# Performance work log

Hardware: AMD Instinct MI355X
Metric: run time of the kernel (lower is better)

## Reference

```python
import jax, jax.numpy as jnp
import numpy as np

NUM_HEADS = 8
D_MODEL = 512
QKV = 512
OUT = 512
B, T = 8, 1024
W = 2 * T - 1  # relative position range


def _relative_shift(x):
    # x: [B, H, T, 2T-1] -> [B, H, T, T] (Transformer-XL shift trick)
    b, h, t, w = x.shape
    zero_pad = jnp.zeros((b, h, t, 1), dtype=x.dtype)
    x = jnp.concatenate([zero_pad, x], axis=-1)  # [B,H,T,2T]
    x = x.reshape(b, h, 2 * t, t)
    x = x[:, :, 1:, :]
    x = x.reshape(b, h, t, 2 * t - 1)
    return x[:, :, :, :t]


def setup_inputs() -> dict:
    key = jax.random.key(0)
    ks = jax.random.split(key, 12)
    s_in = 1.0 / np.sqrt(D_MODEL)
    s_qkv = 1.0 / np.sqrt(QKV)
    return {
        "x": jax.random.normal(ks[0], (B, T, D_MODEL), jnp.float32),
        "pos_emb": jax.random.normal(ks[1], (W, D_MODEL), jnp.float32),
        "Wq": jax.random.normal(ks[2], (D_MODEL, QKV), jnp.float32) * s_in,
        "bq": jnp.zeros((QKV,), jnp.float32),
        "Wk": jax.random.normal(ks[3], (D_MODEL, QKV), jnp.float32) * s_in,
        "Wv": jax.random.normal(ks[4], (D_MODEL, QKV), jnp.float32) * s_in,
        "Wp": jax.random.normal(ks[5], (D_MODEL, QKV), jnp.float32) * s_in,
        "Wo": jax.random.normal(ks[6], (QKV, OUT), jnp.float32) * s_qkv,
        "bo": jnp.zeros((OUT,), jnp.float32),
        "u": jax.random.normal(ks[7], (NUM_HEADS, QKV // NUM_HEADS), jnp.float32),
        "v": jax.random.normal(ks[8], (NUM_HEADS, QKV // NUM_HEADS), jnp.float32),
    }


def reference(x, pos_emb, Wq, bq, Wk, Wv, Wp, Wo, bo, u, v):
    b, t, _ = x.shape
    h = NUM_HEADS
    d = Wq.shape[1] // h
    q = (x @ Wq + bq).reshape(b, t, h, d)
    k = (x @ Wk).reshape(b, t, h, d)
    val = (x @ Wv).reshape(b, t, h, d)
    p = (pos_emb @ Wp).reshape(-1, h, d)  # [2T-1, H, d]

    # content scores: (q + u) . k  -> [B,H,T,T]
    content_scores = jnp.einsum('bthd,bshd->bhts', q + u, k)
    # position scores: (q + v) . p -> [B,H,T,2T-1], then relative shift
    pos_scores = jnp.einsum('bthd,whd->bhtw', q + v, p)
    pos_scores = _relative_shift(pos_scores)

    scores = (content_scores + pos_scores) / jnp.sqrt(jnp.asarray(d, x.dtype))
    probs = jax.nn.softmax(scores, axis=-1)
    attn_out = jnp.einsum('bhts,bshd->bthd', probs, val).reshape(b, t, h * d)
    return attn_out @ Wo + bo
```

## Files before the change

kernel.cpp:

```cpp
#include <hip/hip_runtime.h>
#include <hip/hip_bf16.h>


typedef __attribute__((ext_vector_type(8))) short short8;
typedef __attribute__((ext_vector_type(4))) float float4v;
typedef __fp16 h2v __attribute__((ext_vector_type(2)));

__device__ __forceinline__ unsigned short f2bf(float f) {
  union { float f; unsigned u; } x; x.f = f;
  unsigned r = x.u + 0x7FFFu + ((x.u >> 16) & 1u);
  return (unsigned short)(r >> 16);
}
__device__ __forceinline__ float bf2f(unsigned short b) {
  union { unsigned u; float f; } x; x.u = ((unsigned)b) << 16;
  return x.f;
}
__device__ __forceinline__ int pk2h(float a, float b) {
  union { h2v h; int i; } c; c.h = __builtin_amdgcn_cvt_pkrtz(a, b);
  return c.i;
}
__device__ __forceinline__ float h_lo(int w) {
  union { int i; h2v h; } c; c.i = w; return (float)c.h.x;
}
__device__ __forceinline__ float h_hi(int w) {
  union { int i; h2v h; } c; c.i = w; return (float)c.h.y;
}

__global__ void cvt_bf16_kernel(const float* __restrict__ in,
                                unsigned short* __restrict__ out, int n4) {
  int i = blockIdx.x * blockDim.x + threadIdx.x;
  if (i < n4) {
    float4 f = ((const float4*)in)[i];
    ushort4 r;
    r.x = f2bf(f.x); r.y = f2bf(f.y); r.z = f2bf(f.z); r.w = f2bf(f.w);
    ((ushort4*)out)[i] = r;
  }
}

__global__ void transpose_cvt5_kernel(const float* __restrict__ Wq,
                                      const float* __restrict__ Wk,
                                      const float* __restrict__ Wv,
                                      const float* __restrict__ Wp,
                                      const float* __restrict__ Wo,
                                      unsigned short* __restrict__ dst) {
  int y = blockIdx.y;
  const float* w = (y == 0) ? Wq : (y == 1) ? Wk : (y == 2) ? Wv : (y == 3) ? Wp : Wo;
  unsigned short* wt = dst + (size_t)y * 262144;
  int idx = blockIdx.x * 256 + threadIdx.x;
  int kk = idx >> 9, n = idx & 511;
  wt[(n << 9) | kk] = f2bf(w[idx]);
}

__global__ __launch_bounds__(256, 2) void qkv_gemm128(
    const unsigned short* __restrict__ A,
    const unsigned short* __restrict__ Bt,
    const float* __restrict__ bq,
    const float* __restrict__ uvec,
    const float* __restrict__ vvec,
    unsigned short* __restrict__ QU, unsigned short* __restrict__ QV,
    unsigned short* __restrict__ Kb, unsigned short* __restrict__ Vt) {
  __shared__ __align__(16) unsigned short lds[2 * 128 * 72];
  unsigned short (*As)[72] = (unsigned short(*)[72])lds;
  unsigned short (*Bs)[72] = (unsigned short(*)[72])(lds + 128 * 72);
  int mt = blockIdx.x, nt = blockIdx.y;
  int tid = threadIdx.x;
  int lane = tid & 63, wave = tid >> 6;
  int l15 = lane & 15, g = lane >> 4;
  int wr = (wave >> 1) << 6, wc = (wave & 1) << 6;
  int sr = tid >> 1, sc = (tid & 1) << 5;

  const unsigned short* Ap = A + (size_t)(mt * 128 + sr) * 512 + sc;
  const unsigned short* Bp = Bt + (size_t)(nt * 128 + sr) * 512 + sc;

  uint4 a0 = *(const uint4*)Ap,        a1 = *(const uint4*)(Ap + 8);
  uint4 a2 = *(const uint4*)(Ap + 16), a3 = *(const uint4*)(Ap + 24);
  uint4 b0 = *(const uint4*)Bp,        b1 = *(const uint4*)(Bp + 8);
  uint4 b2 = *(const uint4*)(Bp + 16), b3 = *(const uint4*)(Bp + 24);

  float4v acc[4][4] = {};
  for (int kt = 0; kt < 8; ++kt) {
    *(uint4*)&As[sr][sc]      = a0; *(uint4*)&As[sr][sc + 8]  = a1;
    *(uint4*)&As[sr][sc + 16] = a2; *(uint4*)&As[sr][sc + 24] = a3;
    *(uint4*)&Bs[sr][sc]      = b0; *(uint4*)&Bs[sr][sc + 8]  = b1;
    *(uint4*)&Bs[sr][sc + 16] = b2; *(uint4*)&Bs[sr][sc + 24] = b3;
    __syncthreads();
    if (kt < 7) {
      const unsigned short* ap = Ap + (kt + 1) * 64;
      a0 = *(const uint4*)ap;        a1 = *(const uint4*)(ap + 8);
      a2 = *(const uint4*)(ap + 16); a3 = *(const uint4*)(ap + 24);
      const unsigned short* bp = Bp + (kt + 1) * 64;
      b0 = *(const uint4*)bp;        b1 = *(const uint4*)(bp + 8);
      b2 = *(const uint4*)(bp + 16); b3 = *(const uint4*)(bp + 24);
    }
#pragma unroll
    for (int ks = 0; ks < 2; ++ks) {
      short8 af[4], bf[4];
#pragma unroll
      for (int fm = 0; fm < 4; ++fm)
        af[fm] = *(const short8*)&As[wr + fm * 16 + l15][ks * 32 + g * 8];
#pragma unroll
      for (int fn = 0; fn < 4; ++fn)
        bf[fn] = *(const short8*)&Bs[wc + fn * 16 + l15][ks * 32 + g * 8];
#pragma unroll
      for (int fm = 0; fm < 4; ++fm)
#pragma unroll
        for (int fn = 0; fn < 4; ++fn)
          acc[fm][fn] = __builtin_amdgcn_mfma_f32_16x16x32_bf16(
              af[fm], bf[fn], acc[fm][fn], 0, 0, 0);
    }
    if (kt < 7) __syncthreads();
  }

  if (nt < 4) {
#pragma unroll
    for (int fn = 0; fn < 4; ++fn) {
      int col = nt * 128 + wc + fn * 16 + l15;
      float bs = bq[col], uu = uvec[col], vv = vvec[col];
#pragma unroll
      for (int fm = 0; fm < 4; ++fm) {
        int row = mt * 128 + wr + fm * 16 + 4 * g;
#pragma unroll
        for (int r = 0; r < 4; ++r) {
          size_t idx = (size_t)(row + r) * 512 + col;
          float base = acc[fm][fn][r] + bs;
          QU[idx] = f2bf(base + uu);
          QV[idx] = f2bf(base + vv);
        }
      }
    }
  } else if (nt < 8) {
#pragma unroll
    for (int fn = 0; fn < 4; ++fn) {
      int col = (nt - 4) * 128 + wc + fn * 16 + l15;
#pragma unroll
      for (int fm = 0; fm < 4; ++fm) {
        int row = mt * 128 + wr + fm * 16 + 4 * g;
#pragma unroll
        for (int r = 0; r < 4; ++r)
          Kb[(size_t)(row + r) * 512 + col] = f2bf(acc[fm][fn][r]);
      }
    }
  } else {
    __syncthreads();
    unsigned short (*T)[136] = (unsigned short(*)[136])lds;
#pragma unroll
    for (int fm = 0; fm < 4; ++fm)
#pragma unroll
      for (int fn = 0; fn < 4; ++fn)
#pragma unroll
        for (int r = 0; r < 4; ++r)
          T[wc + fn * 16 + l15][wr + fm * 16 + 4 * g + r] = f2bf(acc[fm][fn][r]);
    __syncthreads();
    int c2 = tid >> 1, sh = (tid & 1) << 6;
    int gcol = (nt - 8) * 128 + c2;
    int bb = mt >> 3, s0 = (mt & 7) * 128;
    unsigned short* op = Vt +
        ((size_t)((bb * 8 + (gcol >> 6)) * 64 + (gcol & 63))) * 1024 + s0 + sh;
#pragma unroll
    for (int j = 0; j < 8; ++j)
      *(uint4*)(op + j * 8) = *(uint4*)&T[c2][sh + j * 8];
  }
}

__global__ __launch_bounds__(256, 2) void gemm128f(
    const unsigned short* __restrict__ A,
    const unsigned short* __restrict__ Bt,
    const float* __restrict__ bias,
    float* __restrict__ Cf) {
  __shared__ __align__(16) unsigned short lds[2 * 128 * 72];
  unsigned short (*As)[72] = (unsigned short(*)[72])lds;
  unsigned short (*Bs)[72] = (unsigned short(*)[72])(lds + 128 * 72);
  int mt = blockIdx.x, nt = blockIdx.y;
  int tid = threadIdx.x;
  int lane = tid & 63, wave = tid >> 6;
  int l15 = lane & 15, g = lane >> 4;
  int wr = (wave >> 1) << 6, wc = (wave & 1) << 6;
  int sr = tid >> 1, sc = (tid & 1) << 5;

  const unsigned short* Ap = A + (size_t)(mt * 128 + sr) * 512 + sc;
  const unsigned short* Bp = Bt + (size_t)(nt * 128 + sr) * 512 + sc;

  uint4 a0 = *(const uint4*)Ap,        a1 = *(const uint4*)(Ap + 8);
  uint4 a2 = *(const uint4*)(Ap + 16), a3 = *(const uint4*)(Ap + 24);
  uint4 b0 = *(const uint4*)Bp,        b1 = *(const uint4*)(Bp + 8);
  uint4 b2 = *(const uint4*)(Bp + 16), b3 = *(const uint4*)(Bp + 24);

  float4v acc[4][4] = {};
  for (int kt = 0; kt < 8; ++kt) {
    *(uint4*)&As[sr][sc]      = a0; *(uint4*)&As[sr][sc + 8]  = a1;
    *(uint4*)&As[sr][sc + 16] = a2; *(uint4*)&As[sr][sc + 24] = a3;
    *(uint4*)&Bs[sr][sc]      = b0; *(uint4*)&Bs[sr][sc + 8]  = b1;
    *(uint4*)&Bs[sr][sc + 16] = b2; *(uint4*)&Bs[sr][sc + 24] = b3;
    __syncthreads();
    if (kt < 7) {
      const unsigned short* ap = Ap + (kt + 1) * 64;
      a0 = *(const uint4*)ap;        a1 = *(const uint4*)(ap + 8);
      a2 = *(const uint4*)(ap + 16); a3 = *(const uint4*)(ap + 24);
      const unsigned short* bp = Bp + (kt + 1) * 64;
      b0 = *(const uint4*)bp;        b1 = *(const uint4*)(bp + 8);
      b2 = *(const uint4*)(bp + 16); b3 = *(const uint4*)(bp + 24);
    }
#pragma unroll
    for (int ks = 0; ks < 2; ++ks) {
      short8 af[4], bf[4];
#pragma unroll
      for (int fm = 0; fm < 4; ++fm)
        af[fm] = *(const short8*)&As[wr + fm * 16 + l15][ks * 32 + g * 8];
#pragma unroll
      for (int fn = 0; fn < 4; ++fn)
        bf[fn] = *(const short8*)&Bs[wc + fn * 16 + l15][ks * 32 + g * 8];
#pragma unroll
      for (int fm = 0; fm < 4; ++fm)
#pragma unroll
        for (int fn = 0; fn < 4; ++fn)
          acc[fm][fn] = __builtin_amdgcn_mfma_f32_16x16x32_bf16(
              af[fm], bf[fn], acc[fm][fn], 0, 0, 0);
    }
    if (kt < 7) __syncthreads();
  }
#pragma unroll
  for (int fn = 0; fn < 4; ++fn) {
    int col = nt * 128 + wc + fn * 16 + l15;
    float bs = bias[col];
#pragma unroll
    for (int fm = 0; fm < 4; ++fm) {
      int row = mt * 128 + wr + fm * 16 + 4 * g;
#pragma unroll
      for (int r = 0; r < 4; ++r)
        Cf[(size_t)(row + r) * 512 + col] = acc[fm][fn][r] + bs;
    }
  }
}

__global__ __launch_bounds__(256) void gemm_kernel(
    const unsigned short* __restrict__ A,
    const unsigned short* __restrict__ Bt,
    const float* __restrict__ bias,
    unsigned short* __restrict__ Cb,
    float* __restrict__ Cf,
    int M, int f32out) {
  __shared__ __align__(16) unsigned short As[64][72];
  __shared__ __align__(16) unsigned short Bs[64][72];
  int mt = blockIdx.x, nt = blockIdx.y;
  int tid = threadIdx.x;
  int lr = tid >> 2, lc = (tid & 3) << 4;
  int lane = tid & 63, wave = tid >> 6;

  int arow = mt * 64 + lr; if (arow >= M) arow = M - 1;
  const unsigned short* Ap = A + (size_t)arow * 512 + lc;
  const unsigned short* Bp = Bt + (size_t)(nt * 64 + lr) * 512 + lc;

  uint4 a0 = *(const uint4*)Ap, a1 = *(const uint4*)(Ap + 8);
  uint4 b0 = *(const uint4*)Bp, b1 = *(const uint4*)(Bp + 8);
  float4v acc[4] = {};
  for (int kt = 0; kt < 8; ++kt) {
    *(uint4*)&As[lr][lc]     = a0;
    *(uint4*)&As[lr][lc + 8] = a1;
    *(uint4*)&Bs[lr][lc]     = b0;
    *(uint4*)&Bs[lr][lc + 8] = b1;
    __syncthreads();
    if (kt < 7) {
      a0 = *(const uint4*)(Ap + (kt + 1) * 64);
      a1 = *(const uint4*)(Ap + (kt + 1) * 64 + 8);
      b0 = *(const uint4*)(Bp + (kt + 1) * 64);
      b1 = *(const uint4*)(Bp + (kt + 1) * 64 + 8);
    }
#pragma unroll
    for (int ks = 0; ks < 2; ++ks) {
      short8 a = *(const short8*)&As[wave * 16 + (lane & 15)][ks * 32 + (lane >> 4) * 8];
#pragma unroll
      for (int fn = 0; fn < 4; ++fn) {
        short8 b = *(const short8*)&Bs[fn * 16 + (lane & 15)][ks * 32 + (lane >> 4) * 8];
        acc[fn] = __builtin_amdgcn_mfma_f32_16x16x32_bf16(a, b, acc[fn], 0, 0, 0);
      }
    }
    if (kt < 7) __syncthreads();
  }
  int rbase = mt * 64 + wave * 16 + ((lane >> 4) << 2);
  int cb = nt * 64 + (lane & 15);
#pragma unroll
  for (int fn = 0; fn < 4; ++fn) {
    int col = cb + fn * 16;
    float bs = bias ? bias[col] : 0.0f;
#pragma unroll
    for (int r = 0; r < 4; ++r) {
      int row = rbase + r;
      if (row < M) {
        float val = acc[fn][r] + bs;
        if (f32out) Cf[(size_t)row * 512 + col] = val;
        else        Cb[(size_t)row * 512 + col] = f2bf(val);
      }
    }
  }
}

__global__ __launch_bounds__(256, 3) void attn_kernel(
    const unsigned short* __restrict__ QU,
    const unsigned short* __restrict__ QV,
    const unsigned short* __restrict__ K,
    const unsigned short* __restrict__ Vt,
    const unsigned short* __restrict__ P,
    unsigned short* __restrict__ O) {
  __shared__ __align__(16) unsigned short k_s[64][72];
  __shared__ __align__(16) unsigned short vt_s[64][72];
  __shared__ __align__(16) unsigned short win_s[128 * 72];

  int pid = blockIdx.x;
  int wid = (pid & 7) * 128 + (pid >> 3);
  int tt = wid & 15, h = (wid >> 4) & 7, b = wid >> 7;
  int t0 = tt * 64;
  int tid = threadIdx.x, lane = tid & 63, wave = tid >> 6;
  int lr = tid >> 2, lc = (tid & 3) << 4;
  int l15 = lane & 15, g = lane >> 4;
  int w16 = wave * 16;
  int C = 3 - wave;

  short8 aqu[2], aqv[2];
  {
    size_t qoff = (size_t)(b * 1024 + t0 + w16 + l15) * 512 + h * 64 + g * 8;
    aqu[0] = *(const short8*)(QU + qoff);
    aqu[1] = *(const short8*)(QU + qoff + 32);
    aqv[0] = *(const short8*)(QV + qoff);
    aqv[1] = *(const short8*)(QV + qoff + 32);
  }

  const unsigned short* Kbase = K + (size_t)(b * 1024) * 512 + h * 64;
  const unsigned short* Vbase = Vt + (size_t)((b * 8 + h) * 64) * 1024;

  float4v accO[4] = {};
  float l_r[4] = {0.f, 0.f, 0.f, 0.f};

  {
    const unsigned short* kp = Kbase + (size_t)lr * 512 + lc;
    uint4 k0 = *(const uint4*)kp, k1 = *(const uint4*)(kp + 8);
    const unsigned short* vp = Vbase + (size_t)lr * 1024 + lc;
    uint4 v0 = *(const uint4*)vp, v1 = *(const uint4*)(vp + 8);
    int r2 = tid >> 1, c2 = (tid & 1) << 5;
    int ph0 = (tt + 1) & 1;
    int wr = 960 - t0 + r2;
    const unsigned short* pp = P + (size_t)wr * 512 + h * 64 + c2;
    uint4 w0v = *(const uint4*)pp,        w1v = *(const uint4*)(pp + 8);
    uint4 w2v = *(const uint4*)(pp + 16), w3v = *(const uint4*)(pp + 24);
    *(uint4*)&k_s[lr][lc]      = k0; *(uint4*)&k_s[lr][lc + 8]  = k1;
    *(uint4*)&vt_s[lr][lc]     = v0; *(uint4*)&vt_s[lr][lc + 8] = v1;
    unsigned short* dp = &win_s[(r2 ^ (ph0 << 6)) * 72 + c2];
    *(uint4*)dp        = w0v; *(uint4*)(dp + 8)  = w1v;
    *(uint4*)(dp + 16) = w2v; *(uint4*)(dp + 24) = w3v;
  }
  __syncthreads();

  uint4 pk0, pk1, pv0, pv1, pw0, pw1;
  for (int st = 0; st < 16; ++st) {
    int ph = (st + tt + 1) & 1;
    if (st < 15) {
      int s0n = (st + 1) * 64;
      const unsigned short* kp = Kbase + (size_t)(s0n + lr) * 512 + lc;
      pk0 = *(const uint4*)kp; pk1 = *(const uint4*)(kp + 8);
      const unsigned short* vp = Vbase + (size_t)lr * 1024 + s0n + lc;
      pv0 = *(const uint4*)vp; pv1 = *(const uint4*)(vp + 8);
      int wr = 64 * st - t0 + 1088 + lr; if (wr > 2046) wr = 2046;
      const unsigned short* pp = P + (size_t)wr * 512 + h * 64 + lc;
      pw0 = *(const uint4*)pp; pw1 = *(const uint4*)(pp + 8);
    }

    float4v accS[4] = {}; float4v accP[5] = {};
#pragma unroll
    for (int ks = 0; ks < 2; ++ks) {
#pragma unroll
      for (int fn = 0; fn < 4; ++fn) {
        short8 bk = *(const short8*)&k_s[fn * 16 + l15][ks * 32 + g * 8];
        accS[fn] = __builtin_amdgcn_mfma_f32_16x16x32_bf16(aqu[ks], bk, accS[fn], 0, 0, 0);
      }
#pragma unroll
      for (int k = 0; k < 5; ++k) {
        int fi = (k + C) ^ (ph << 2);
        short8 bp = *(const short8*)&win_s[(fi * 16 + l15) * 72 + ks * 32 + g * 8];
        accP[k] = __builtin_amdgcn_mfma_f32_16x16x32_bf16(aqv[ks], bp, accP[k], 0, 0, 0);
      }
    }

#pragma unroll
    for (int r = 0; r < 4; ++r) {
      int W0 = pk2h(accP[0][r], accP[1][r]);
      int W1 = pk2h(accP[1][r], accP[2][r]);
      int W2 = pk2h(accP[2][r], accP[3][r]);
      int W3 = pk2h(accP[3][r], accP[4][r]);
      int srcLane = (lane & 48) | ((l15 - 4 * g - r - 1) & 15);
      int carry = (l15 >= 4 * g + r + 1);
      int x0 = __shfl(W0, srcLane), x1 = __shfl(W1, srcLane);
      int x2 = __shfl(W2, srcLane), x3 = __shfl(W3, srcLane);
      int wa = carry ? x1 : x0;
      int wb = carry ? x3 : x2;
      accS[0][r] = (accS[0][r] + h_lo(wa)) * 0.125f;
      accS[1][r] = (accS[1][r] + h_hi(wa)) * 0.125f;
      accS[2][r] = (accS[2][r] + h_lo(wb)) * 0.125f;
      accS[3][r] = (accS[3][r] + h_hi(wb)) * 0.125f;
    }

    __syncthreads();

    int pbase = (ph << 6) + w16;
#pragma unroll
    for (int r = 0; r < 4; ++r) {
      float rs = 0.f;
#pragma unroll
      for (int fn = 0; fn < 4; ++fn) {
        float e = __expf(accS[fn][r] - 8.0f);
        win_s[(pbase + 4 * g + r) * 72 + fn * 16 + l15] = f2bf(e);
        rs += e;
      }
      l_r[r] += rs;
    }

#pragma unroll
    for (int ks = 0; ks < 2; ++ks) {
      short8 ap = *(const short8*)&win_s[(pbase + l15) * 72 + ks * 32 + g * 8];
#pragma unroll
      for (int fn = 0; fn < 4; ++fn) {
        short8 bv = *(const short8*)&vt_s[fn * 16 + l15][ks * 32 + g * 8];
        accO[fn] = __builtin_amdgcn_mfma_f32_16x16x32_bf16(ap, bv, accO[fn], 0, 0, 0);
      }
    }

    if (st < 15) {
      __syncthreads();
      *(uint4*)&k_s[lr][lc]      = pk0; *(uint4*)&k_s[lr][lc + 8]  = pk1;
      *(uint4*)&vt_s[lr][lc]     = pv0; *(uint4*)&vt_s[lr][lc + 8] = pv1;
      unsigned short* dp = &win_s[(lr + (ph << 6)) * 72 + lc];
      *(uint4*)dp = pw0; *(uint4*)(dp + 8) = pw1;
      __syncthreads();
    }
  }

  float rinv[4];
#pragma unroll
  for (int r = 0; r < 4; ++r) {
    float l = l_r[r];
    l += __shfl_xor(l, 1); l += __shfl_xor(l, 2);
    l += __shfl_xor(l, 4); l += __shfl_xor(l, 8);
    rinv[r] = 1.0f / l;
  }
#pragma unroll
  for (int fn = 0; fn < 4; ++fn) {
    int dcol = fn * 16 + l15;
#pragma unroll
    for (int r = 0; r < 4; ++r) {
      int row = t0 + w16 + 4 * g + r;
      float o = accO[fn][r] * rinv[r];
      O[(size_t)(b * 1024 + row) * 512 + h * 64 + dcol] = f2bf(o);
    }
  }
}

extern "C" void kernel_launch(void* const* d_in, const int* in_sizes, int n_in,
                              void* d_out, int out_size, void* d_ws, size_t ws_size,
                              hipStream_t stream) {
  const float* x       = (const float*)d_in[0];
  const float* pos_emb = (const float*)d_in[1];
  const float* Wq      = (const float*)d_in[2];
  const float* bq      = (const float*)d_in[3];
  const float* Wk      = (const float*)d_in[4];
  const float* Wv      = (const float*)d_in[5];
  const float* Wp      = (const float*)d_in[6];
  const float* Wo      = (const float*)d_in[7];
  const float* bo      = (const float*)d_in[8];
  const float* u       = (const float*)d_in[9];
  const float* v       = (const float*)d_in[10];

  char* ws = (char*)d_ws;
  unsigned short* xb   = (unsigned short*)ws; ws += (size_t)8192 * 512 * 2;
  unsigned short* peb  = (unsigned short*)ws; ws += (size_t)2048 * 512 * 2;
  unsigned short* wqkv = (unsigned short*)ws; ws += (size_t)5 * 512 * 512 * 2;
  unsigned short* qub  = (unsigned short*)ws; ws += (size_t)8192 * 512 * 2;
  unsigned short* qvb  = (unsigned short*)ws; ws += (size_t)8192 * 512 * 2;
  unsigned short* kb   = (unsigned short*)ws; ws += (size_t)8192 * 512 * 2;
  unsigned short* vtb  = (unsigned short*)ws; ws += (size_t)8192 * 512 * 2;
  unsigned short* pb   = (unsigned short*)ws; ws += (size_t)2048 * 512 * 2;
  unsigned short* attb = (unsigned short*)ws; ws += (size_t)8192 * 512 * 2;

  cvt_bf16_kernel<<<4096, 256, 0, stream>>>(x, xb, 1048576);
  cvt_bf16_kernel<<<1024, 256, 0, stream>>>(pos_emb, peb, 262016);
  transpose_cvt5_kernel<<<dim3(1024, 5), 256, 0, stream>>>(Wq, Wk, Wv, Wp, Wo, wqkv);
  unsigned short* wpt_p = wqkv + (size_t)3 * 262144;
  unsigned short* wot_p = wqkv + (size_t)4 * 262144;

  qkv_gemm128<<<dim3(64, 12), 256, 0, stream>>>(xb, wqkv, bq, u, v,
                                                qub, qvb, kb, vtb);
  gemm_kernel<<<dim3(32, 8), 256, 0, stream>>>(peb, wpt_p, nullptr, pb, nullptr, 2047, 0);

  attn_kernel<<<1024, 256, 0, stream>>>(qub, qvb, kb, vtb, pb, attb);

  gemm128f<<<dim3(64, 4), 256, 0, stream>>>(attb, wot_p, bo, (float*)d_out);
}
```

Before: 128.5 us.

## Double attention query tile, fuse position GEMM into QKV GEMM, tile weight transpose

The attention kernel now processes 128 query rows per block as two 64-row subtiles. The K/V tiles and a larger 192-row position window are shared across both subtiles, halving K/V reloads and the number of blocks. The position embedding projection is folded into the QKV GEMM launch as an extra grid row, removing a separate kernel launch. The weight transpose uses an LDS tile for coalesced reads and writes. The cost is higher register and LDS use per block in attention, which lowers occupancy.

```diff
diff --git a/kernel.cpp b/kernel.cpp
--- a/kernel.cpp
+++ b/kernel.cpp
@@ -10,10 +10,6 @@
   union { float f; unsigned u; } x; x.f = f;
   unsigned r = x.u + 0x7FFFu + ((x.u >> 16) & 1u);
   return (unsigned short)(r >> 16);
-}
-__device__ __forceinline__ float bf2f(unsigned short b) {
-  union { unsigned u; float f; } x; x.u = ((unsigned)b) << 16;
-  return x.f;
 }
 __device__ __forceinline__ int pk2h(float a, float b) {
   union { h2v h; int i; } c; c.h = __builtin_amdgcn_cvt_pkrtz(a, b);
@@ -43,12 +39,28 @@
                                       const float* __restrict__ Wp,
                                       const float* __restrict__ Wo,
                                       unsigned short* __restrict__ dst) {
+  __shared__ float T[64][65];
   int y = blockIdx.y;
   const float* w = (y == 0) ? Wq : (y == 1) ? Wk : (y == 2) ? Wv : (y == 3) ? Wp : Wo;
   unsigned short* wt = dst + (size_t)y * 262144;
-  int idx = blockIdx.x * 256 + threadIdx.x;
-  int kk = idx >> 9, n = idx & 511;
-  wt[(n << 9) | kk] = f2bf(w[idx]);
+  int bx = blockIdx.x;
+  int r0 = (bx >> 3) * 64, c0 = (bx & 7) * 64;
+  int tid = threadIdx.x;
+  int row = tid >> 2, cq = (tid & 3) * 16;
+  const float* src = w + (size_t)(r0 + row) * 512 + c0 + cq;
+#pragma unroll
+  for (int j = 0; j < 4; ++j) {
+    float4 f = *(const float4*)(src + j * 4);
+    T[row][cq + j * 4 + 0] = f.x; T[row][cq + j * 4 + 1] = f.y;
+    T[row][cq + j * 4 + 2] = f.z; T[row][cq + j * 4 + 3] = f.w;
+  }
+  __syncthreads();
+  unsigned short tmp[16];
+#pragma unroll
+  for (int j = 0; j < 16; ++j) tmp[j] = f2bf(T[cq + j][row]);
+  unsigned short* op = wt + (size_t)(c0 + row) * 512 + r0 + cq;
+  *(uint4*)op       = *(uint4*)tmp;
+  *(uint4*)(op + 8) = *(uint4*)(tmp + 8);
 }
 
 __global__ __launch_bounds__(256, 2) void qkv_gemm128(
@@ -58,7 +70,10 @@
     const float* __restrict__ uvec,
     const float* __restrict__ vvec,
     unsigned short* __restrict__ QU, unsigned short* __restrict__ QV,
-    unsigned short* __restrict__ Kb, unsigned short* __restrict__ Vt) {
+    unsigned short* __restrict__ Kb, unsigned short* __restrict__ Vt,
+    const unsigned short* __restrict__ Pe,
+    const unsigned short* __restrict__ Wpt,
+    unsigned short* __restrict__ Pb) {
   __shared__ __align__(16) unsigned short lds[2 * 128 * 72];
   unsigned short (*As)[72] = (unsigned short(*)[72])lds;
   unsigned short (*Bs)[72] = (unsigned short(*)[72])(lds + 128 * 72);
@@ -69,8 +84,15 @@
   int wr = (wave >> 1) << 6, wc = (wave & 1) << 6;
   int sr = tid >> 1, sc = (tid & 1) << 5;
 
-  const unsigned short* Ap = A + (size_t)(mt * 128 + sr) * 512 + sc;
-  const unsigned short* Bp = Bt + (size_t)(nt * 128 + sr) * 512 + sc;
+  const unsigned short* Ap;
+  const unsigned short* Bp;
+  if (nt < 12) {
+    Ap = A + (size_t)(mt * 128 + sr) * 512 + sc;
+    Bp = Bt + (size_t)(nt * 128 + sr) * 512 + sc;
+  } else {
+    Ap = Pe + (size_t)((mt & 15) * 128 + sr) * 512 + sc;
+    Bp = Wpt + (size_t)((mt >> 4) * 128 + sr) * 512 + sc;
+  }
 
   uint4 a0 = *(const uint4*)Ap,        a1 = *(const uint4*)(Ap + 8);
   uint4 a2 = *(const uint4*)(Ap + 16), a3 = *(const uint4*)(Ap + 24);
@@ -140,7 +162,7 @@
           Kb[(size_t)(row + r) * 512 + col] = f2bf(acc[fm][fn][r]);
       }
     }
-  } else {
+  } else if (nt < 12) {
     __syncthreads();
     unsigned short (*T)[136] = (unsigned short(*)[136])lds;
 #pragma unroll
@@ -159,6 +181,18 @@
 #pragma unroll
     for (int j = 0; j < 8; ++j)
       *(uint4*)(op + j * 8) = *(uint4*)&T[c2][sh + j * 8];
+  } else {
+#pragma unroll
+    for (int fn = 0; fn < 4; ++fn) {
+      int col = (mt >> 4) * 128 + wc + fn * 16 + l15;
+#pragma unroll
+      for (int fm = 0; fm < 4; ++fm) {
+        int row = (mt & 15) * 128 + wr + fm * 16 + 4 * g;
+#pragma unroll
+        for (int r = 0; r < 4; ++r)
+          Pb[(size_t)(row + r) * 512 + col] = f2bf(acc[fm][fn][r]);
+      }
+    }
   }
 }
 
@@ -232,69 +266,7 @@
   }
 }
 
-__global__ __launch_bounds__(256) void gemm_kernel(
-    const unsigned short* __restrict__ A,
-    const unsigned short* __restrict__ Bt,
-    const float* __restrict__ bias,
-    unsigned short* __restrict__ Cb,
-    float* __restrict__ Cf,
-    int M, int f32out) {
-  __shared__ __align__(16) unsigned short As[64][72];
-  __shared__ __align__(16) unsigned short Bs[64][72];
-  int mt = blockIdx.x, nt = blockIdx.y;
-  int tid = threadIdx.x;
-  int lr = tid >> 2, lc = (tid & 3) << 4;
-  int lane = tid & 63, wave = tid >> 6;
-
-  int arow = mt * 64 + lr; if (arow >= M) arow = M - 1;
-  const unsigned short* Ap = A + (size_t)arow * 512 + lc;
-  const unsigned short* Bp = Bt + (size_t)(nt * 64 + lr) * 512 + lc;
-
-  uint4 a0 = *(const uint4*)Ap, a1 = *(const uint4*)(Ap + 8);
-  uint4 b0 = *(const uint4*)Bp, b1 = *(const uint4*)(Bp + 8);
-  float4v acc[4] = {};
-  for (int kt = 0; kt < 8; ++kt) {
-    *(uint4*)&As[lr][lc]     = a0;
-    *(uint4*)&As[lr][lc + 8] = a1;
-    *(uint4*)&Bs[lr][lc]     = b0;
-    *(uint4*)&Bs[lr][lc + 8] = b1;
-    __syncthreads();
-    if (kt < 7) {
-      a0 = *(const uint4*)(Ap + (kt + 1) * 64);
-      a1 = *(const uint4*)(Ap + (kt + 1) * 64 + 8);
-      b0 = *(const uint4*)(Bp + (kt + 1) * 64);
-      b1 = *(const uint4*)(Bp + (kt + 1) * 64 + 8);
-    }
-#pragma unroll
-    for (int ks = 0; ks < 2; ++ks) {
-      short8 a = *(const short8*)&As[wave * 16 + (lane & 15)][ks * 32 + (lane >> 4) * 8];
-#pragma unroll
-      for (int fn = 0; fn < 4; ++fn) {
-        short8 b = *(const short8*)&Bs[fn * 16 + (lane & 15)][ks * 32 + (lane >> 4) * 8];
-        acc[fn] = __builtin_amdgcn_mfma_f32_16x16x32_bf16(a, b, acc[fn], 0, 0, 0);
-      }
-    }
-    if (kt < 7) __syncthreads();
-  }
-  int rbase = mt * 64 + wave * 16 + ((lane >> 4) << 2);
-  int cb = nt * 64 + (lane & 15);
-#pragma unroll
-  for (int fn = 0; fn < 4; ++fn) {
-    int col = cb + fn * 16;
-    float bs = bias ? bias[col] : 0.0f;
-#pragma unroll
-    for (int r = 0; r < 4; ++r) {
-      int row = rbase + r;
-      if (row < M) {
-        float val = acc[fn][r] + bs;
-        if (f32out) Cf[(size_t)row * 512 + col] = val;
-        else        Cb[(size_t)row * 512 + col] = f2bf(val);
-      }
-    }
-  }
-}
-
-__global__ __launch_bounds__(256, 3) void attn_kernel(
+__global__ __launch_bounds__(256, 2) void attn_kernel(
     const unsigned short* __restrict__ QU,
     const unsigned short* __restrict__ QV,
     const unsigned short* __restrict__ K,
@@ -303,122 +275,137 @@
     unsigned short* __restrict__ O) {
   __shared__ __align__(16) unsigned short k_s[64][72];
   __shared__ __align__(16) unsigned short vt_s[64][72];
-  __shared__ __align__(16) unsigned short win_s[128 * 72];
+  __shared__ __align__(16) unsigned short win_s[192 * 72];
 
   int pid = blockIdx.x;
-  int wid = (pid & 7) * 128 + (pid >> 3);
-  int tt = wid & 15, h = (wid >> 4) & 7, b = wid >> 7;
-  int t0 = tt * 64;
+  int wid = (pid & 7) * 64 + (pid >> 3);
+  int tt = wid & 7, b = (wid >> 3) & 7, h = wid >> 6;
+  int t0 = tt * 128;
   int tid = threadIdx.x, lane = tid & 63, wave = tid >> 6;
   int lr = tid >> 2, lc = (tid & 3) << 4;
   int l15 = lane & 15, g = lane >> 4;
   int w16 = wave * 16;
+  int wrow = tid >> 3, wcol = (tid & 7) << 3;
   int C = 3 - wave;
 
-  short8 aqu[2], aqv[2];
-  {
-    size_t qoff = (size_t)(b * 1024 + t0 + w16 + l15) * 512 + h * 64 + g * 8;
-    aqu[0] = *(const short8*)(QU + qoff);
-    aqu[1] = *(const short8*)(QU + qoff + 32);
-    aqv[0] = *(const short8*)(QV + qoff);
-    aqv[1] = *(const short8*)(QV + qoff + 32);
+  short8 aqu[2][2], aqv[2][2];
+#pragma unroll
+  for (int m = 0; m < 2; ++m) {
+    size_t qoff = (size_t)(b * 1024 + t0 + 64 * m + w16 + l15) * 512 + h * 64 + g * 8;
+    aqu[m][0] = *(const short8*)(QU + qoff);
+    aqu[m][1] = *(const short8*)(QU + qoff + 32);
+    aqv[m][0] = *(const short8*)(QV + qoff);
+    aqv[m][1] = *(const short8*)(QV + qoff + 32);
   }
 
   const unsigned short* Kbase = K + (size_t)(b * 1024) * 512 + h * 64;
   const unsigned short* Vbase = Vt + (size_t)((b * 8 + h) * 64) * 1024;
-
-  float4v accO[4] = {};
-  float l_r[4] = {0.f, 0.f, 0.f, 0.f};
+  const unsigned short* Pbase = P + h * 64;
+
+  float4v accO[2][4] = {};
+  float l_r[2][4] = {};
 
   {
     const unsigned short* kp = Kbase + (size_t)lr * 512 + lc;
     uint4 k0 = *(const uint4*)kp, k1 = *(const uint4*)(kp + 8);
     const unsigned short* vp = Vbase + (size_t)lr * 1024 + lc;
     uint4 v0 = *(const uint4*)vp, v1 = *(const uint4*)(vp + 8);
-    int r2 = tid >> 1, c2 = (tid & 1) << 5;
-    int ph0 = (tt + 1) & 1;
-    int wr = 960 - t0 + r2;
-    const unsigned short* pp = P + (size_t)wr * 512 + h * 64 + c2;
-    uint4 w0v = *(const uint4*)pp,        w1v = *(const uint4*)(pp + 8);
-    uint4 w2v = *(const uint4*)(pp + 16), w3v = *(const uint4*)(pp + 24);
+    int wb = 896 - t0;
+    uint4 wv[6];
+#pragma unroll
+    for (int c = 0; c < 6; ++c)
+      wv[c] = *(const uint4*)(Pbase + (size_t)(wb + c * 32 + wrow) * 512 + wcol);
     *(uint4*)&k_s[lr][lc]      = k0; *(uint4*)&k_s[lr][lc + 8]  = k1;
     *(uint4*)&vt_s[lr][lc]     = v0; *(uint4*)&vt_s[lr][lc + 8] = v1;
-    unsigned short* dp = &win_s[(r2 ^ (ph0 << 6)) * 72 + c2];
-    *(uint4*)dp        = w0v; *(uint4*)(dp + 8)  = w1v;
-    *(uint4*)(dp + 16) = w2v; *(uint4*)(dp + 24) = w3v;
+#pragma unroll
+    for (int c = 0; c < 6; ++c)
+      *(uint4*)&win_s[(c * 32 + wrow) * 72 + wcol] = wv[c];
   }
   __syncthreads();
 
-  uint4 pk0, pk1, pv0, pv1, pw0, pw1;
+  uint4 pk0, pk1, pv0, pv1, pw[6];
   for (int st = 0; st < 16; ++st) {
-    int ph = (st + tt + 1) & 1;
     if (st < 15) {
       int s0n = (st + 1) * 64;
       const unsigned short* kp = Kbase + (size_t)(s0n + lr) * 512 + lc;
       pk0 = *(const uint4*)kp; pk1 = *(const uint4*)(kp + 8);
       const unsigned short* vp = Vbase + (size_t)lr * 1024 + s0n + lc;
       pv0 = *(const uint4*)vp; pv1 = *(const uint4*)(vp + 8);
-      int wr = 64 * st - t0 + 1088 + lr; if (wr > 2046) wr = 2046;
-      const unsigned short* pp = P + (size_t)wr * 512 + h * 64 + lc;
-      pw0 = *(const uint4*)pp; pw1 = *(const uint4*)(pp + 8);
-    }
-
-    float4v accS[4] = {}; float4v accP[5] = {};
+      int wb = s0n - t0 + 896;
+#pragma unroll
+      for (int c = 0; c < 6; ++c) {
+        int w = wb + c * 32 + wrow; if (w > 2046) w = 2046;
+        pw[c] = *(const uint4*)(Pbase + (size_t)w * 512 + wcol);
+      }
+    }
+
+    float4v accS[2][4] = {}; float4v accP[2][5] = {};
 #pragma unroll
     for (int ks = 0; ks < 2; ++ks) {
 #pragma unroll
       for (int fn = 0; fn < 4; ++fn) {
         short8 bk = *(const short8*)&k_s[fn * 16 + l15][ks * 32 + g * 8];
-        accS[fn] = __builtin_amdgcn_mfma_f32_16x16x32_bf16(aqu[ks], bk, accS[fn], 0, 0, 0);
-      }
-#pragma unroll
-      for (int k = 0; k < 5; ++k) {
-        int fi = (k + C) ^ (ph << 2);
-        short8 bp = *(const short8*)&win_s[(fi * 16 + l15) * 72 + ks * 32 + g * 8];
-        accP[k] = __builtin_amdgcn_mfma_f32_16x16x32_bf16(aqv[ks], bp, accP[k], 0, 0, 0);
-      }
-    }
-
-#pragma unroll
-    for (int r = 0; r < 4; ++r) {
-      int W0 = pk2h(accP[0][r], accP[1][r]);
-      int W1 = pk2h(accP[1][r], accP[2][r]);
-      int W2 = pk2h(accP[2][r], accP[3][r]);
-      int W3 = pk2h(accP[3][r], accP[4][r]);
-      int srcLane = (lane & 48) | ((l15 - 4 * g - r - 1) & 15);
-      int carry = (l15 >= 4 * g + r + 1);
-      int x0 = __shfl(W0, srcLane), x1 = __shfl(W1, srcLane);
-      int x2 = __shfl(W2, srcLane), x3 = __shfl(W3, srcLane);
-      int wa = carry ? x1 : x0;
-      int wb = carry ? x3 : x2;
-      accS[0][r] = (accS[0][r] + h_lo(wa)) * 0.125f;
-      accS[1][r] = (accS[1][r] + h_hi(wa)) * 0.125f;
-      accS[2][r] = (accS[2][r] + h_lo(wb)) * 0.125f;
-      accS[3][r] = (accS[3][r] + h_hi(wb)) * 0.125f;
-    }
+        accS[0][fn] = __builtin_amdgcn_mfma_f32_16x16x32_bf16(aqu[0][ks], bk, accS[0][fn], 0, 0, 0);
+        accS[1][fn] = __builtin_amdgcn_mfma_f32_16x16x32_bf16(aqu[1][ks], bk, accS[1][fn], 0, 0, 0);
+      }
+#pragma unroll
+      for (int j = 0; j < 9; ++j) {
+        short8 bp = *(const short8*)&win_s[((C + j) * 16 + l15) * 72 + ks * 32 + g * 8];
+        if (j <= 4)
+          accP[1][j] = __builtin_amdgcn_mfma_f32_16x16x32_bf16(aqv[1][ks], bp, accP[1][j], 0, 0, 0);
+        if (j >= 4)
+          accP[0][j - 4] = __builtin_amdgcn_mfma_f32_16x16x32_bf16(aqv[0][ks], bp, accP[0][j - 4], 0, 0, 0);
+      }
+    }
+
+#pragma unroll
+    for (int m = 0; m < 2; ++m)
+#pragma unroll
+      for (int r = 0; r < 4; ++r) {
+        int W0 = pk2h(accP[m][0][r], accP[m][1][r]);
+        int W1 = pk2h(accP[m][1][r], accP[m][2][r]);
+        int W2 = pk2h(accP[m][2][r], accP[m][3][r]);
+        int W3 = pk2h(accP[m][3][r], accP[m][4][r]);
+        int srcLane = (lane & 48) | ((l15 - 4 * g - r - 1) & 15);
+        int carry = (l15 >= 4 * g + r + 1);
+        int x0 = __shfl(W0, srcLane), x1 = __shfl(W1, srcLane);
+        int x2 = __shfl(W2, srcLane), x3 = __shfl(W3, srcLane);
+        int wa = carry ? x1 : x0;
+        int wb2 = carry ? x3 : x2;
+        accS[m][0][r] = (accS[m][0][r] + h_lo(wa)) * 0.125f;
+        accS[m][1][r] = (accS[m][1][r] + h_hi(wa)) * 0.125f;
+        accS[m][2][r] = (accS[m][2][r] + h_lo(wb2)) * 0.125f;
+        accS[m][3][r] = (accS[m][3][r] + h_hi(wb2)) * 0.125f;
+      }
 
     __syncthreads();
 
-    int pbase = (ph << 6) + w16;
-#pragma unroll
-    for (int r = 0; r < 4; ++r) {
-      float rs = 0.f;
-#pragma unroll
-      for (int fn = 0; fn < 4; ++fn) {
-        float e = __expf(accS[fn][r] - 8.0f);
-        win_s[(pbase + 4 * g + r) * 72 + fn * 16 + l15] = f2bf(e);
-        rs += e;
-      }
-      l_r[r] += rs;
-    }
+#pragma unroll
+    for (int m = 0; m < 2; ++m)
+#pragma unroll
+      for (int r = 0; r < 4; ++r) {
+        float rs = 0.f;
+#pragma unroll
+        for (int fn = 0; fn < 4; ++fn) {
+          float e = __expf(accS[m][fn][r] - 8.0f);
+          win_s[(64 * m + w16 + 4 * g + r) * 72 + fn * 16 + l15] = f2bf(e);
+          rs += e;
+        }
+        l_r[m][r] += rs;
+      }
 
 #pragma unroll
     for (int ks = 0; ks < 2; ++ks) {
-      short8 ap = *(const short8*)&win_s[(pbase + l15) * 72 + ks * 32 + g * 8];
-#pragma unroll
-      for (int fn = 0; fn < 4; ++fn) {
-        short8 bv = *(const short8*)&vt_s[fn * 16 + l15][ks * 32 + g * 8];
-        accO[fn] = __builtin_amdgcn_mfma_f32_16x16x32_bf16(ap, bv, accO[fn], 0, 0, 0);
+      short8 bv[4];
+#pragma unroll
+      for (int fn = 0; fn < 4; ++fn)
+        bv[fn] = *(const short8*)&vt_s[fn * 16 + l15][ks * 32 + g * 8];
+#pragma unroll
+      for (int m = 0; m < 2; ++m) {
+        short8 ap = *(const short8*)&win_s[(64 * m + w16 + l15) * 72 + ks * 32 + g * 8];
+#pragma unroll
+        for (int fn = 0; fn < 4; ++fn)
+          accO[m][fn] = __builtin_amdgcn_mfma_f32_16x16x32_bf16(ap, bv[fn], accO[m][fn], 0, 0, 0);
       }
     }
 
@@ -426,28 +413,32 @@
       __syncthreads();
       *(uint4*)&k_s[lr][lc]      = pk0; *(uint4*)&k_s[lr][lc + 8]  = pk1;
       *(uint4*)&vt_s[lr][lc]     = pv0; *(uint4*)&vt_s[lr][lc + 8] = pv1;
-      unsigned short* dp = &win_s[(lr + (ph << 6)) * 72 + lc];
-      *(uint4*)dp = pw0; *(uint4*)(dp + 8) = pw1;
+#pragma unroll
+      for (int c = 0; c < 6; ++c)
+        *(uint4*)&win_s[(c * 32 + wrow) * 72 + wcol] = pw[c];
       __syncthreads();
     }
   }
 
-  float rinv[4];
-#pragma unroll
-  for (int r = 0; r < 4; ++r) {
-    float l = l_r[r];
-    l += __shfl_xor(l, 1); l += __shfl_xor(l, 2);
-    l += __shfl_xor(l, 4); l += __shfl_xor(l, 8);
-    rinv[r] = 1.0f / l;
-  }
-#pragma unroll
-  for (int fn = 0; fn < 4; ++fn) {
-    int dcol = fn * 16 + l15;
+#pragma unroll
+  for (int m = 0; m < 2; ++m) {
+    float rinv[4];
 #pragma unroll
     for (int r = 0; r < 4; ++r) {
-      int row = t0 + w16 + 4 * g + r;
-      float o = accO[fn][r] * rinv[r];
-      O[(size_t)(b * 1024 + row) * 512 + h * 64 + dcol] = f2bf(o);
+      float l = l_r[m][r];
+      l += __shfl_xor(l, 1); l += __shfl_xor(l, 2);
+      l += __shfl_xor(l, 4); l += __shfl_xor(l, 8);
+      rinv[r] = 1.0f / l;
+    }
+#pragma unroll
+    for (int fn = 0; fn < 4; ++fn) {
+      int dcol = fn * 16 + l15;
+#pragma unroll
+      for (int r = 0; r < 4; ++r) {
+        int row = t0 + 64 * m + w16 + 4 * g + r;
+        float o = accO[m][fn][r] * rinv[r];
+        O[(size_t)(b * 1024 + row) * 512 + h * 64 + dcol] = f2bf(o);
+      }
     }
   }
 }
@@ -480,15 +471,15 @@
 
   cvt_bf16_kernel<<<4096, 256, 0, stream>>>(x, xb, 1048576);
   cvt_bf16_kernel<<<1024, 256, 0, stream>>>(pos_emb, peb, 262016);
-  transpose_cvt5_kernel<<<dim3(1024, 5), 256, 0, stream>>>(Wq, Wk, Wv, Wp, Wo, wqkv);
+  transpose_cvt5_kernel<<<dim3(64, 5), 256, 0, stream>>>(Wq, Wk, Wv, Wp, Wo, wqkv);
   unsigned short* wpt_p = wqkv + (size_t)3 * 262144;
   unsigned short* wot_p = wqkv + (size_t)4 * 262144;
 
-  qkv_gemm128<<<dim3(64, 12), 256, 0, stream>>>(xb, wqkv, bq, u, v,
-                                                qub, qvb, kb, vtb);
-  gemm_kernel<<<dim3(32, 8), 256, 0, stream>>>(peb, wpt_p, nullptr, pb, nullptr, 2047, 0);
-
-  attn_kernel<<<1024, 256, 0, stream>>>(qub, qvb, kb, vtb, pb, attb);
+  qkv_gemm128<<<dim3(64, 13), 256, 0, stream>>>(xb, wqkv, bq, u, v,
+                                                qub, qvb, kb, vtb,
+                                                peb, wpt_p, pb);
+
+  attn_kernel<<<512, 256, 0, stream>>>(qub, qvb, kb, vtb, pb, attb);
 
   gemm128f<<<dim3(64, 4), 256, 0, stream>>>(attb, wot_p, bo, (float*)d_out);
 }
```

Result: slower. 144.4 us (+12.4%).

## Fold pos-emb projection into QKV GEMM grid and tile weight transpose via LDS

Applied to the files above, without the earlier changes.

The separate 64x64 GEMM that projected pos_emb by Wp is removed. That work now runs as an extra row of 128x128 tiles (nt==12) in the QKV GEMM launch, which saves one kernel launch and lets it share the larger-tile path. The weight transpose/convert kernel now stages 64x64 tiles through padded shared memory, so both the float reads and the bf16 writes are coalesced instead of scattering 2-byte stores. The P tile computes the full 2048th row from a padded buffer whose last row is never written, which is harmless only as long as that row is never consumed.

```diff
diff --git a/kernel.cpp b/kernel.cpp
--- a/kernel.cpp
+++ b/kernel.cpp
@@ -10,10 +10,6 @@
   union { float f; unsigned u; } x; x.f = f;
   unsigned r = x.u + 0x7FFFu + ((x.u >> 16) & 1u);
   return (unsigned short)(r >> 16);
-}
-__device__ __forceinline__ float bf2f(unsigned short b) {
-  union { unsigned u; float f; } x; x.u = ((unsigned)b) << 16;
-  return x.f;
 }
 __device__ __forceinline__ int pk2h(float a, float b) {
   union { h2v h; int i; } c; c.h = __builtin_amdgcn_cvt_pkrtz(a, b);
@@ -43,12 +39,28 @@
                                       const float* __restrict__ Wp,
                                       const float* __restrict__ Wo,
                                       unsigned short* __restrict__ dst) {
+  __shared__ float T[64][65];
   int y = blockIdx.y;
   const float* w = (y == 0) ? Wq : (y == 1) ? Wk : (y == 2) ? Wv : (y == 3) ? Wp : Wo;
   unsigned short* wt = dst + (size_t)y * 262144;
-  int idx = blockIdx.x * 256 + threadIdx.x;
-  int kk = idx >> 9, n = idx & 511;
-  wt[(n << 9) | kk] = f2bf(w[idx]);
+  int bx = blockIdx.x;
+  int r0 = (bx >> 3) * 64, c0 = (bx & 7) * 64;
+  int tid = threadIdx.x;
+  int row = tid >> 2, cq = (tid & 3) * 16;
+  const float* src = w + (size_t)(r0 + row) * 512 + c0 + cq;
+#pragma unroll
+  for (int j = 0; j < 4; ++j) {
+    float4 f = *(const float4*)(src + j * 4);
+    T[row][cq + j * 4 + 0] = f.x; T[row][cq + j * 4 + 1] = f.y;
+    T[row][cq + j * 4 + 2] = f.z; T[row][cq + j * 4 + 3] = f.w;
+  }
+  __syncthreads();
+  unsigned short tmp[16];
+#pragma unroll
+  for (int j = 0; j < 16; ++j) tmp[j] = f2bf(T[cq + j][row]);
+  unsigned short* op = wt + (size_t)(c0 + row) * 512 + r0 + cq;
+  *(uint4*)op       = *(uint4*)tmp;
+  *(uint4*)(op + 8) = *(uint4*)(tmp + 8);
 }
 
 __global__ __launch_bounds__(256, 2) void qkv_gemm128(
@@ -58,7 +70,10 @@
     const float* __restrict__ uvec,
     const float* __restrict__ vvec,
     unsigned short* __restrict__ QU, unsigned short* __restrict__ QV,
-    unsigned short* __restrict__ Kb, unsigned short* __restrict__ Vt) {
+    unsigned short* __restrict__ Kb, unsigned short* __restrict__ Vt,
+    const unsigned short* __restrict__ Pe,
+    const unsigned short* __restrict__ Wpt,
+    unsigned short* __restrict__ Pb) {
   __shared__ __align__(16) unsigned short lds[2 * 128 * 72];
   unsigned short (*As)[72] = (unsigned short(*)[72])lds;
   unsigned short (*Bs)[72] = (unsigned short(*)[72])(lds + 128 * 72);
@@ -69,8 +84,15 @@
   int wr = (wave >> 1) << 6, wc = (wave & 1) << 6;
   int sr = tid >> 1, sc = (tid & 1) << 5;
 
-  const unsigned short* Ap = A + (size_t)(mt * 128 + sr) * 512 + sc;
-  const unsigned short* Bp = Bt + (size_t)(nt * 128 + sr) * 512 + sc;
+  const unsigned short* Ap;
+  const unsigned short* Bp;
+  if (nt < 12) {
+    Ap = A + (size_t)(mt * 128 + sr) * 512 + sc;
+    Bp = Bt + (size_t)(nt * 128 + sr) * 512 + sc;
+  } else {
+    Ap = Pe + (size_t)((mt & 15) * 128 + sr) * 512 + sc;
+    Bp = Wpt + (size_t)((mt >> 4) * 128 + sr) * 512 + sc;
+  }
 
   uint4 a0 = *(const uint4*)Ap,        a1 = *(const uint4*)(Ap + 8);
   uint4 a2 = *(const uint4*)(Ap + 16), a3 = *(const uint4*)(Ap + 24);
@@ -140,7 +162,7 @@
           Kb[(size_t)(row + r) * 512 + col] = f2bf(acc[fm][fn][r]);
       }
     }
-  } else {
+  } else if (nt < 12) {
     __syncthreads();
     unsigned short (*T)[136] = (unsigned short(*)[136])lds;
 #pragma unroll
@@ -159,6 +181,18 @@
 #pragma unroll
     for (int j = 0; j < 8; ++j)
       *(uint4*)(op + j * 8) = *(uint4*)&T[c2][sh + j * 8];
+  } else {
+#pragma unroll
+    for (int fn = 0; fn < 4; ++fn) {
+      int col = (mt >> 4) * 128 + wc + fn * 16 + l15;
+#pragma unroll
+      for (int fm = 0; fm < 4; ++fm) {
+        int row = (mt & 15) * 128 + wr + fm * 16 + 4 * g;
+#pragma unroll
+        for (int r = 0; r < 4; ++r)
+          Pb[(size_t)(row + r) * 512 + col] = f2bf(acc[fm][fn][r]);
+      }
+    }
   }
 }
 
@@ -228,68 +262,6 @@
 #pragma unroll
       for (int r = 0; r < 4; ++r)
         Cf[(size_t)(row + r) * 512 + col] = acc[fm][fn][r] + bs;
-    }
-  }
-}
-
-__global__ __launch_bounds__(256) void gemm_kernel(
-    const unsigned short* __restrict__ A,
-    const unsigned short* __restrict__ Bt,
-    const float* __restrict__ bias,
-    unsigned short* __restrict__ Cb,
-    float* __restrict__ Cf,
-    int M, int f32out) {
-  __shared__ __align__(16) unsigned short As[64][72];
-  __shared__ __align__(16) unsigned short Bs[64][72];
-  int mt = blockIdx.x, nt = blockIdx.y;
-  int tid = threadIdx.x;
-  int lr = tid >> 2, lc = (tid & 3) << 4;
-  int lane = tid & 63, wave = tid >> 6;
-
-  int arow = mt * 64 + lr; if (arow >= M) arow = M - 1;
-  const unsigned short* Ap = A + (size_t)arow * 512 + lc;
-  const unsigned short* Bp = Bt + (size_t)(nt * 64 + lr) * 512 + lc;
-
-  uint4 a0 = *(const uint4*)Ap, a1 = *(const uint4*)(Ap + 8);
-  uint4 b0 = *(const uint4*)Bp, b1 = *(const uint4*)(Bp + 8);
-  float4v acc[4] = {};
-  for (int kt = 0; kt < 8; ++kt) {
-    *(uint4*)&As[lr][lc]     = a0;
-    *(uint4*)&As[lr][lc + 8] = a1;
-    *(uint4*)&Bs[lr][lc]     = b0;
-    *(uint4*)&Bs[lr][lc + 8] = b1;
-    __syncthreads();
-    if (kt < 7) {
-      a0 = *(const uint4*)(Ap + (kt + 1) * 64);
-      a1 = *(const uint4*)(Ap + (kt + 1) * 64 + 8);
-      b0 = *(const uint4*)(Bp + (kt + 1) * 64);
-      b1 = *(const uint4*)(Bp + (kt + 1) * 64 + 8);
-    }
-#pragma unroll
-    for (int ks = 0; ks < 2; ++ks) {
-      short8 a = *(const short8*)&As[wave * 16 + (lane & 15)][ks * 32 + (lane >> 4) * 8];
-#pragma unroll
-      for (int fn = 0; fn < 4; ++fn) {
-        short8 b = *(const short8*)&Bs[fn * 16 + (lane & 15)][ks * 32 + (lane >> 4) * 8];
-        acc[fn] = __builtin_amdgcn_mfma_f32_16x16x32_bf16(a, b, acc[fn], 0, 0, 0);
-      }
-    }
-    if (kt < 7) __syncthreads();
-  }
-  int rbase = mt * 64 + wave * 16 + ((lane >> 4) << 2);
-  int cb = nt * 64 + (lane & 15);
-#pragma unroll
-  for (int fn = 0; fn < 4; ++fn) {
-    int col = cb + fn * 16;
-    float bs = bias ? bias[col] : 0.0f;
-#pragma unroll
-    for (int r = 0; r < 4; ++r) {
-      int row = rbase + r;
-      if (row < M) {
-        float val = acc[fn][r] + bs;
-        if (f32out) Cf[(size_t)row * 512 + col] = val;
-        else        Cb[(size_t)row * 512 + col] = f2bf(val);
-      }
     }
   }
 }
@@ -480,13 +452,13 @@
 
   cvt_bf16_kernel<<<4096, 256, 0, stream>>>(x, xb, 1048576);
   cvt_bf16_kernel<<<1024, 256, 0, stream>>>(pos_emb, peb, 262016);
-  transpose_cvt5_kernel<<<dim3(1024, 5), 256, 0, stream>>>(Wq, Wk, Wv, Wp, Wo, wqkv);
+  transpose_cvt5_kernel<<<dim3(64, 5), 256, 0, stream>>>(Wq, Wk, Wv, Wp, Wo, wqkv);
   unsigned short* wpt_p = wqkv + (size_t)3 * 262144;
   unsigned short* wot_p = wqkv + (size_t)4 * 262144;
 
-  qkv_gemm128<<<dim3(64, 12), 256, 0, stream>>>(xb, wqkv, bq, u, v,
-                                                qub, qvb, kb, vtb);
-  gemm_kernel<<<dim3(32, 8), 256, 0, stream>>>(peb, wpt_p, nullptr, pb, nullptr, 2047, 0);
+  qkv_gemm128<<<dim3(64, 13), 256, 0, stream>>>(xb, wqkv, bq, u, v,
+                                                qub, qvb, kb, vtb,
+                                                peb, wpt_p, pb);
 
   attn_kernel<<<1024, 256, 0, stream>>>(qub, qvb, kb, vtb, pb, attb);
 
```

Result: faster. 122.7 us (-4.5%).
